# Performance work log

Measured on AMD Instinct MI355X. Metric: run time of the kernel, lower is better.

The kernel has to match this reference:

```python
import jax, jax.numpy as jnp
import numpy as np

NX, NY = 8, 1
IN_DELAY, FB_DELAY = 3, 3
MAX_DELAY = max(IN_DELAY, FB_DELAY)
HID = 64
NT, NG = 4096, 1024
IN_FEAT = (NX - NY) * (IN_DELAY + 1) + NY * (FB_DELAY + 1)  # 32


def setup_inputs() -> dict:
    key = jax.random.key(0)
    ks = jax.random.split(key, 10)
    s = lambda *sh: 0.05
    return {
        "x": jax.random.normal(ks[0], (NT, NG, NX), jnp.float32),
        "W_in": jax.random.normal(ks[1], (HID, IN_FEAT), jnp.float32) * 0.1,
        "b_in": jax.random.normal(ks[2], (HID,), jnp.float32) * 0.1,
        "W_ih": jax.random.normal(ks[3], (HID, HID), jnp.float32) * 0.1,
        "b_ih": jax.random.normal(ks[4], (HID,), jnp.float32) * 0.1,
        "W_hh": jax.random.normal(ks[5], (HID, HID), jnp.float32) * 0.1,
        "b_hh": jax.random.normal(ks[6], (HID,), jnp.float32) * 0.1,
        "W_out": jax.random.normal(ks[7], (NY, HID), jnp.float32) * 0.1,
        "b_out": jax.random.normal(ks[8], (NY,), jnp.float32) * 0.1,
    }


def _narx_forward(x, W_in, b_in, W_ih, b_ih, b_hh, W_out, b_out):
    nt = x.shape[0]
    # Source concat order: x0_t = x0[-1] then all x0[i], i=0..delay-1 (last slice duplicated).
    # x0 spans times [t-delay, t-1], so offsets relative to t are:
    off_x = jnp.array([-1] + list(range(-IN_DELAY, 0)))   # [4]
    off_y = jnp.array([-1] + list(range(-FB_DELAY, 0)))   # [4]
    ts = jnp.arange(MAX_DELAY, nt)                          # [T']
    # Gather delay windows: [T', n_off, ngrid, feat] -> [T', ngrid, n_off*feat]
    xw = x[ts[:, None] + off_x[None, :], :, :NX - NY]
    xw = jnp.transpose(xw, (0, 2, 1, 3)).reshape(xw.shape[0], xw.shape[2], -1)
    yw = x[ts[:, None] + off_y[None, :], :, NX - NY:]
    yw = jnp.transpose(yw, (0, 2, 1, 3)).reshape(yw.shape[0], yw.shape[2], -1)
    xt = jnp.concatenate([xw, yw], axis=-1)                 # [T', ngrid, IN_FEAT]
    h = jax.nn.relu(jnp.einsum('tgi,hi->tgh', xt, W_in) + b_in)
    # RNNCell called with hx=None each step in the source -> hidden is zeros every
    # call (W_hh contributes nothing); out = tanh(W_ih h + b_ih + b_hh).
    a = jnp.tanh(jnp.einsum('tgh,oh->tgo', h, W_ih) + b_ih + b_hh)
    y = jnp.einsum('tgh,oh->tgo', a, W_out) + b_out         # [T', ngrid, NY]
    # out[:max_delay] = x[:max_delay, :, -ny:]
    return jnp.concatenate([x[:MAX_DELAY, :, NX - NY:], y], axis=0)


def reference(x, W_in, b_in, W_ih, b_ih, W_hh, b_hh, W_out, b_out):
    # NestedNarx applies the shared Narx dl_model to every basin's series; with
    # the batched Narx this is exactly one call over all basins.
    return _narx_forward(x, W_in, b_in, W_ih, b_ih, b_hh, W_out, b_out)
```

## Files before the change

### kernel.cpp

```cpp
#include <hip/hip_runtime.h>
#include <hip/hip_bf16.h>


typedef __attribute__((ext_vector_type(8))) short bf16x8;
typedef __attribute__((ext_vector_type(4))) float f32x4;

__device__ __forceinline__ unsigned pk2(float lo, float hi) {
    __hip_bfloat162 h = __float22bfloat162_rn(float2{lo, hi});
    unsigned u; __builtin_memcpy(&u, &h, 4);
    return u;
}

union BF8 { bf16x8 v; unsigned u[4]; uint4 q; };


__global__ __launch_bounds__(64) void narx_prep(
    const float* __restrict__ W_in, const float* __restrict__ b_in,
    const float* __restrict__ W_ih, const float* __restrict__ b_ih,
    const float* __restrict__ b_hh, const float* __restrict__ W_out,
    uint4* __restrict__ ws)
{
    const int lane = threadIdx.x;
    const int c = lane >> 4, pl = lane & 15;

    #pragma unroll
    for (int T = 0; T < 4; ++T) {
        const int r = ((pl >> 2) * 8) + (pl & 3) + (T & 1) * 4 + (T >> 1) * 32;
        const float* W = W_in + r * 32;
        float wr[8];
        if (c == 0) {
            #pragma unroll
            for (int j = 0; j < 7; ++j) wr[j] = W[j] + W[21 + j];
            wr[7] = W[28] + W[31];
        } else if (c == 1) {
            #pragma unroll
            for (int j = 0; j < 7; ++j) wr[j] = W[14 + j];
            wr[7] = W[30];
        } else if (c == 2) {
            #pragma unroll
            for (int j = 0; j < 7; ++j) wr[j] = W[7 + j];
            wr[7] = W[29];
        } else {
            wr[0] = b_in[r];
            #pragma unroll
            for (int j = 1; j < 8; ++j) wr[j] = 0.0f;
        }
        BF8 t;
        t.u[0] = pk2(wr[0], wr[1]); t.u[1] = pk2(wr[2], wr[3]);
        t.u[2] = pk2(wr[4], wr[5]); t.u[3] = pk2(wr[6], wr[7]);
        ws[lane*4 + T] = t.q;
    }

    #pragma unroll
    for (int k0 = 0; k0 < 2; ++k0)
    #pragma unroll
    for (int U = 0; U < 4; ++U) {
        const int r = ((pl >> 2) * 8) + (pl & 3) + (U & 1) * 4 + (U >> 1) * 32;
        const float* p = W_ih + r * 64 + 32*k0 + 8*c;
        float4 u0 = *(const float4*)p, u1 = *(const float4*)(p + 4);
        BF8 t;
        t.u[0] = pk2(u0.x, u0.y); t.u[1] = pk2(u0.z, u0.w);
        t.u[2] = pk2(u1.x, u1.y); t.u[3] = pk2(u1.z, u1.w);
        ws[256 + lane*8 + k0*4 + U] = t.q;
    }

    float* bsum = (float*)&ws[1536];
    if (lane < 64) {  }
    float4* wsf = (float4*)ws;
    #pragma unroll
    for (int U = 0; U < 4; ++U) {
        const int o = 8*c + 4*(U & 1) + 32*(U >> 1);
        wsf[768 + lane*4 + U] = make_float4(b_ih[o+0]+b_hh[o+0], b_ih[o+1]+b_hh[o+1],
                                            b_ih[o+2]+b_hh[o+2], b_ih[o+3]+b_hh[o+3]);
    }
    (void)bsum;

    #pragma unroll
    for (int k0 = 0; k0 < 2; ++k0) {
        BF8 t;
        if (pl == 0) {
            const float* p = W_out + 32*k0 + 8*c;
            t.u[0] = pk2(p[0], p[1]); t.u[1] = pk2(p[2], p[3]);
            t.u[2] = pk2(p[4], p[5]); t.u[3] = pk2(p[6], p[7]);
        } else {
            t.u[0] = t.u[1] = t.u[2] = t.u[3] = 0u;
        }
        ws[1280 + lane*2 + k0] = t.q;
    }
}

__global__ __launch_bounds__(256, 2) void narx_main(
    const float* __restrict__ x, const uint4* __restrict__ ws,
    const float* __restrict__ b_out, float* __restrict__ out)
{
    __shared__ unsigned short F[4][128][32];

    const int nwg  = gridDim.x;
    const int orig = blockIdx.x;
    const int q8 = nwg >> 3, r8 = nwg & 7;
    const int xcd = orig & 7, inner = orig >> 3;
    const int b = (xcd < r8 ? xcd * (q8 + 1) : r8 * (q8 + 1) + (xcd - r8) * q8) + inner;

    const int lane = threadIdx.x & 63;
    const int w    = threadIdx.x >> 6;
    const int c    = lane >> 4;
    const int pl   = lane & 15;
    const int pt0  = 3072 + b * 512 + w * 128;

    bf16x8 wa[4];
    #pragma unroll
    for (int T = 0; T < 4; ++T) { BF8 t; t.q = ws[lane*4 + T]; wa[T] = t.v; }
    bf16x8 wi[2][4];
    #pragma unroll
    for (int k0 = 0; k0 < 2; ++k0)
    #pragma unroll
    for (int U = 0; U < 4; ++U) { BF8 t; t.q = ws[256 + lane*8 + k0*4 + U]; wi[k0][U] = t.v; }
    bf16x8 woa[2];
    #pragma unroll
    for (int k0 = 0; k0 < 2; ++k0) { BF8 t; t.q = ws[1280 + lane*2 + k0]; woa[k0] = t.v; }
    const float4* wsf = (const float4*)ws;
    f32x4 bias2[4];
    #pragma unroll
    for (int U = 0; U < 4; ++U) {
        float4 v = wsf[768 + lane*4 + U];
        bias2[U] = f32x4{v.x, v.y, v.z, v.w};
    }
    const float bout = b_out[0];
    const f32x4 cy = {c == 0 ? bout : 0.f, 0.f, 0.f, 0.f};
    const f32x4 zero = {0.f, 0.f, 0.f, 0.f};

    const float4* xr = (const float4*)x;
    {
        const int p0 = pt0 + lane, p1 = pt0 + 64 + lane;
        const int t0 = p0 >> 10, g0v = p0 & 1023;
        const int t1 = p1 >> 10, g1v = p1 & 1023;
        const size_t a1 = ((size_t)(t0-1)*1024 + g0v)*2, a2 = ((size_t)(t0-2)*1024 + g0v)*2,
                     a3 = ((size_t)(t0-3)*1024 + g0v)*2;
        const size_t d1a = ((size_t)(t1-1)*1024 + g1v)*2, d2a = ((size_t)(t1-2)*1024 + g1v)*2,
                     d3a = ((size_t)(t1-3)*1024 + g1v)*2;
        float4 A0 = xr[a1],  A1 = xr[a1+1],  B0 = xr[a2],  B1 = xr[a2+1],
               C0 = xr[a3],  C1 = xr[a3+1];
        float4 D0 = xr[d1a], D1 = xr[d1a+1], E0 = xr[d2a], E1 = xr[d2a+1],
               G0 = xr[d3a], G1 = xr[d3a+1];
        const int s = (lane >> 1) & 3;
        uint4* Fr0 = (uint4*)&F[w][lane][0];
        Fr0[0 ^ s] = make_uint4(pk2(A0.x,A0.y), pk2(A0.z,A0.w), pk2(A1.x,A1.y), pk2(A1.z,A1.w));
        Fr0[1 ^ s] = make_uint4(pk2(B0.x,B0.y), pk2(B0.z,B0.w), pk2(B1.x,B1.y), pk2(B1.z,B1.w));
        Fr0[2 ^ s] = make_uint4(pk2(C0.x,C0.y), pk2(C0.z,C0.w), pk2(C1.x,C1.y), pk2(C1.z,C1.w));
        Fr0[3 ^ s] = make_uint4(0x00003f80u, 0u, 0u, 0u);
        uint4* Fr1 = (uint4*)&F[w][64 + lane][0];
        Fr1[0 ^ s] = make_uint4(pk2(D0.x,D0.y), pk2(D0.z,D0.w), pk2(D1.x,D1.y), pk2(D1.z,D1.w));
        Fr1[1 ^ s] = make_uint4(pk2(E0.x,E0.y), pk2(E0.z,E0.w), pk2(E1.x,E1.y), pk2(E1.z,E1.w));
        Fr1[2 ^ s] = make_uint4(pk2(G0.x,G0.y), pk2(G0.z,G0.w), pk2(G1.x,G1.y), pk2(G1.z,G1.w));
        Fr1[3 ^ s] = make_uint4(0x00003f80u, 0u, 0u, 0u);
    }
    asm volatile("s_waitcnt lgkmcnt(0)" ::: "memory");
    __builtin_amdgcn_sched_barrier(0);

    asm volatile("" : "+v"(wa[0]), "+v"(wa[1]), "+v"(wa[2]), "+v"(wa[3]),
                      "+v"(wi[0][0]), "+v"(wi[0][1]), "+v"(wi[0][2]), "+v"(wi[0][3]),
                      "+v"(wi[1][0]), "+v"(wi[1][1]), "+v"(wi[1][2]), "+v"(wi[1][3]),
                      "+v"(bias2[0]), "+v"(bias2[1]), "+v"(bias2[2]), "+v"(bias2[3]),
                      "+v"(woa[0]), "+v"(woa[1]));

    const int s_rd = (pl >> 1) & 3;
    bf16x8 bf1 = *(bf16x8*)&F[w][pl][(c ^ s_rd) * 8];

    #pragma unroll 2
    for (int rb = 0; rb < 8; ++rb) {
        const int m0 = pt0 + rb * 16;

        f32x4 d1[4];
        #pragma unroll
        for (int T = 0; T < 4; ++T)
            d1[T] = __builtin_amdgcn_mfma_f32_16x16x32_bf16(wa[T], bf1, zero, 0, 0, 0);

        {
            const int rn = (rb < 7) ? rb + 1 : 7;
            bf1 = *(bf16x8*)&F[w][rn*16 + pl][(c ^ s_rd) * 8];
        }

        BF8 bh0, bh1;
        bh0.u[0] = pk2(fmaxf(d1[0][0],0.f), fmaxf(d1[0][1],0.f));
        bh0.u[1] = pk2(fmaxf(d1[0][2],0.f), fmaxf(d1[0][3],0.f));
        bh0.u[2] = pk2(fmaxf(d1[1][0],0.f), fmaxf(d1[1][1],0.f));
        bh0.u[3] = pk2(fmaxf(d1[1][2],0.f), fmaxf(d1[1][3],0.f));
        bh1.u[0] = pk2(fmaxf(d1[2][0],0.f), fmaxf(d1[2][1],0.f));
        bh1.u[1] = pk2(fmaxf(d1[2][2],0.f), fmaxf(d1[2][3],0.f));
        bh1.u[2] = pk2(fmaxf(d1[3][0],0.f), fmaxf(d1[3][1],0.f));
        bh1.u[3] = pk2(fmaxf(d1[3][2],0.f), fmaxf(d1[3][3],0.f));

        f32x4 d2[4];
        #pragma unroll
        for (int U = 0; U < 4; ++U) {
            d2[U] = __builtin_amdgcn_mfma_f32_16x16x32_bf16(wi[0][U], bh0.v, bias2[U], 0, 0, 0);
            d2[U] = __builtin_amdgcn_mfma_f32_16x16x32_bf16(wi[1][U], bh1.v, d2[U],   0, 0, 0);
        }

        f32x4 av[4];
        #pragma unroll
        for (int U = 0; U < 4; ++U) {
            f32x4 z;
            z[0] = __builtin_amdgcn_fmed3f(d2[U][0], -4.f, 4.f);
            z[1] = __builtin_amdgcn_fmed3f(d2[U][1], -4.f, 4.f);
            z[2] = __builtin_amdgcn_fmed3f(d2[U][2], -4.f, 4.f);
            z[3] = __builtin_amdgcn_fmed3f(d2[U][3], -4.f, 4.f);
            f32x4 p2  = z * z;
            f32x4 num = z * (p2 * (p2 + 105.f) + 945.f);
            f32x4 den = p2 * (p2 * 15.f + 420.f) + 945.f;
            f32x4 r;
            r[0] = __builtin_amdgcn_rcpf(den[0]);
            r[1] = __builtin_amdgcn_rcpf(den[1]);
            r[2] = __builtin_amdgcn_rcpf(den[2]);
            r[3] = __builtin_amdgcn_rcpf(den[3]);
            av[U] = num * r;
        }
        BF8 pb0, pb1;
        pb0.u[0] = pk2(av[0][0], av[0][1]); pb0.u[1] = pk2(av[0][2], av[0][3]);
        pb0.u[2] = pk2(av[1][0], av[1][1]); pb0.u[3] = pk2(av[1][2], av[1][3]);
        pb1.u[0] = pk2(av[2][0], av[2][1]); pb1.u[1] = pk2(av[2][2], av[2][3]);
        pb1.u[2] = pk2(av[3][0], av[3][1]); pb1.u[3] = pk2(av[3][2], av[3][3]);

        f32x4 dy;
        dy = __builtin_amdgcn_mfma_f32_16x16x32_bf16(woa[0], pb0.v, cy, 0, 0, 0);
        dy = __builtin_amdgcn_mfma_f32_16x16x32_bf16(woa[1], pb1.v, dy, 0, 0, 0);

        if (lane < 16)
            out[m0 + lane] = dy[0];
    }
}

__global__ __launch_bounds__(256) void narx_pass(const float* __restrict__ x, float* __restrict__ out) {
    const int i = blockIdx.x * 256 + threadIdx.x;
    out[i] = x[i * 8 + 7];
}

extern "C" void kernel_launch(void* const* d_in, const int* in_sizes, int n_in,
                              void* d_out, int out_size, void* d_ws, size_t ws_size,
                              hipStream_t stream) {
    const float* x     = (const float*)d_in[0];
    const float* W_in  = (const float*)d_in[1];
    const float* b_in  = (const float*)d_in[2];
    const float* W_ih  = (const float*)d_in[3];
    const float* b_ih  = (const float*)d_in[4];
    const float* b_hh  = (const float*)d_in[6];
    const float* W_out = (const float*)d_in[7];
    const float* b_out = (const float*)d_in[8];
    float* out = (float*)d_out;
    uint4* ws = (uint4*)d_ws;

    narx_prep<<<1, 64, 0, stream>>>(W_in, b_in, W_ih, b_ih, b_hh, W_out, ws);
    narx_main<<<8186, 256, 0, stream>>>(x, ws, b_out, out);
    narx_pass<<<12, 256, 0, stream>>>(x, out);
}
```

Baseline: 128.8 us.

## Load MFMA B-operands directly from global into registers, drop LDS staging; relu via abs trick

Removes the shared-memory staging buffer: each lane now loads its delayed-input slices straight from global memory into registers, software-prefetched four row-blocks ahead, and packs them into the bf16 B operand inline. ReLU is rewritten as 0.5*(h+|h|): W_ih is prescaled by 0.5 and the second layer runs twice as many MFMAs, once on h and once on |h|, replacing the max operations. Dropping LDS and raising the occupancy hint to 3 waves aims to hide latency better, at the cost of doubled second-layer matrix work and less coalesced, partly redundant global loads.

```diff
diff --git a/kernel.cpp b/kernel.cpp
--- a/kernel.cpp
+++ b/kernel.cpp
@@ -59,13 +59,11 @@
         const float* p = W_ih + r * 64 + 32*k0 + 8*c;
         float4 u0 = *(const float4*)p, u1 = *(const float4*)(p + 4);
         BF8 t;
-        t.u[0] = pk2(u0.x, u0.y); t.u[1] = pk2(u0.z, u0.w);
-        t.u[2] = pk2(u1.x, u1.y); t.u[3] = pk2(u1.z, u1.w);
+        t.u[0] = pk2(0.5f*u0.x, 0.5f*u0.y); t.u[1] = pk2(0.5f*u0.z, 0.5f*u0.w);
+        t.u[2] = pk2(0.5f*u1.x, 0.5f*u1.y); t.u[3] = pk2(0.5f*u1.z, 0.5f*u1.w);
         ws[256 + lane*8 + k0*4 + U] = t.q;
     }
 
-    float* bsum = (float*)&ws[1536];
-    if (lane < 64) {  }
     float4* wsf = (float4*)ws;
     #pragma unroll
     for (int U = 0; U < 4; ++U) {
@@ -73,7 +71,6 @@
         wsf[768 + lane*4 + U] = make_float4(b_ih[o+0]+b_hh[o+0], b_ih[o+1]+b_hh[o+1],
                                             b_ih[o+2]+b_hh[o+2], b_ih[o+3]+b_hh[o+3]);
     }
-    (void)bsum;
 
     #pragma unroll
     for (int k0 = 0; k0 < 2; ++k0) {
@@ -89,12 +86,10 @@
     }
 }
 
-__global__ __launch_bounds__(256, 2) void narx_main(
+__global__ __launch_bounds__(256, 3) void narx_main(
     const float* __restrict__ x, const uint4* __restrict__ ws,
     const float* __restrict__ b_out, float* __restrict__ out)
 {
-    __shared__ unsigned short F[4][128][32];
-
     const int nwg  = gridDim.x;
     const int orig = blockIdx.x;
     const int q8 = nwg >> 3, r8 = nwg & 7;
@@ -129,72 +124,68 @@
     const f32x4 cy = {c == 0 ? bout : 0.f, 0.f, 0.f, 0.f};
     const f32x4 zero = {0.f, 0.f, 0.f, 0.f};
 
-    const float4* xr = (const float4*)x;
-    {
-        const int p0 = pt0 + lane, p1 = pt0 + 64 + lane;
-        const int t0 = p0 >> 10, g0v = p0 & 1023;
-        const int t1 = p1 >> 10, g1v = p1 & 1023;
-        const size_t a1 = ((size_t)(t0-1)*1024 + g0v)*2, a2 = ((size_t)(t0-2)*1024 + g0v)*2,
-                     a3 = ((size_t)(t0-3)*1024 + g0v)*2;
-        const size_t d1a = ((size_t)(t1-1)*1024 + g1v)*2, d2a = ((size_t)(t1-2)*1024 + g1v)*2,
-                     d3a = ((size_t)(t1-3)*1024 + g1v)*2;
-        float4 A0 = xr[a1],  A1 = xr[a1+1],  B0 = xr[a2],  B1 = xr[a2+1],
-               C0 = xr[a3],  C1 = xr[a3+1];
-        float4 D0 = xr[d1a], D1 = xr[d1a+1], E0 = xr[d2a], E1 = xr[d2a+1],
-               G0 = xr[d3a], G1 = xr[d3a+1];
-        const int s = (lane >> 1) & 3;
-        uint4* Fr0 = (uint4*)&F[w][lane][0];
-        Fr0[0 ^ s] = make_uint4(pk2(A0.x,A0.y), pk2(A0.z,A0.w), pk2(A1.x,A1.y), pk2(A1.z,A1.w));
-        Fr0[1 ^ s] = make_uint4(pk2(B0.x,B0.y), pk2(B0.z,B0.w), pk2(B1.x,B1.y), pk2(B1.z,B1.w));
-        Fr0[2 ^ s] = make_uint4(pk2(C0.x,C0.y), pk2(C0.z,C0.w), pk2(C1.x,C1.y), pk2(C1.z,C1.w));
-        Fr0[3 ^ s] = make_uint4(0x00003f80u, 0u, 0u, 0u);
-        uint4* Fr1 = (uint4*)&F[w][64 + lane][0];
-        Fr1[0 ^ s] = make_uint4(pk2(D0.x,D0.y), pk2(D0.z,D0.w), pk2(D1.x,D1.y), pk2(D1.z,D1.w));
-        Fr1[1 ^ s] = make_uint4(pk2(E0.x,E0.y), pk2(E0.z,E0.w), pk2(E1.x,E1.y), pk2(E1.z,E1.w));
-        Fr1[2 ^ s] = make_uint4(pk2(G0.x,G0.y), pk2(G0.z,G0.w), pk2(G1.x,G1.y), pk2(G1.z,G1.w));
-        Fr1[3 ^ s] = make_uint4(0x00003f80u, 0u, 0u, 0u);
-    }
-    asm volatile("s_waitcnt lgkmcnt(0)" ::: "memory");
-    __builtin_amdgcn_sched_barrier(0);
-
     asm volatile("" : "+v"(wa[0]), "+v"(wa[1]), "+v"(wa[2]), "+v"(wa[3]),
                       "+v"(wi[0][0]), "+v"(wi[0][1]), "+v"(wi[0][2]), "+v"(wi[0][3]),
                       "+v"(wi[1][0]), "+v"(wi[1][1]), "+v"(wi[1][2]), "+v"(wi[1][3]),
                       "+v"(bias2[0]), "+v"(bias2[1]), "+v"(bias2[2]), "+v"(bias2[3]),
                       "+v"(woa[0]), "+v"(woa[1]));
 
-    const int s_rd = (pl >> 1) & 3;
-    bf16x8 bf1 = *(bf16x8*)&F[w][pl][(c ^ s_rd) * 8];
-
-    #pragma unroll 2
+    const int t  = pt0 >> 10, g0 = pt0 & 1023;
+    const int dly = (c < 3) ? c : 0;
+    const float* xb = x + ((size_t)(t - 1 - dly) * 1024 + g0 + pl) * 8;
+    float4 L0[4], L1[4];
+    if (c < 3) {
+        #pragma unroll
+        for (int i = 0; i < 4; ++i) {
+            const float4* p = (const float4*)(xb + i * 128);
+            L0[i] = p[0]; L1[i] = p[1];
+        }
+    }
+
+    #pragma unroll
     for (int rb = 0; rb < 8; ++rb) {
         const int m0 = pt0 + rb * 16;
 
+        bf16x8 bf1;
+        {
+            BF8 tv;
+            if (c < 3) {
+                float4 a = L0[rb & 3], bq = L1[rb & 3];
+                tv.u[0] = pk2(a.x, a.y);  tv.u[1] = pk2(a.z, a.w);
+                tv.u[2] = pk2(bq.x, bq.y); tv.u[3] = pk2(bq.z, bq.w);
+            } else {
+                tv.u[0] = 0x00003f80u; tv.u[1] = 0u; tv.u[2] = 0u; tv.u[3] = 0u;
+            }
+            bf1 = tv.v;
+        }
+
         f32x4 d1[4];
         #pragma unroll
         for (int T = 0; T < 4; ++T)
             d1[T] = __builtin_amdgcn_mfma_f32_16x16x32_bf16(wa[T], bf1, zero, 0, 0, 0);
 
-        {
-            const int rn = (rb < 7) ? rb + 1 : 7;
-            bf1 = *(bf16x8*)&F[w][rn*16 + pl][(c ^ s_rd) * 8];
-        }
-
-        BF8 bh0, bh1;
-        bh0.u[0] = pk2(fmaxf(d1[0][0],0.f), fmaxf(d1[0][1],0.f));
-        bh0.u[1] = pk2(fmaxf(d1[0][2],0.f), fmaxf(d1[0][3],0.f));
-        bh0.u[2] = pk2(fmaxf(d1[1][0],0.f), fmaxf(d1[1][1],0.f));
-        bh0.u[3] = pk2(fmaxf(d1[1][2],0.f), fmaxf(d1[1][3],0.f));
-        bh1.u[0] = pk2(fmaxf(d1[2][0],0.f), fmaxf(d1[2][1],0.f));
-        bh1.u[1] = pk2(fmaxf(d1[2][2],0.f), fmaxf(d1[2][3],0.f));
-        bh1.u[2] = pk2(fmaxf(d1[3][0],0.f), fmaxf(d1[3][1],0.f));
-        bh1.u[3] = pk2(fmaxf(d1[3][2],0.f), fmaxf(d1[3][3],0.f));
+        if (rb < 4 && c < 3) {
+            const float4* p = (const float4*)(xb + (rb + 4) * 128);
+            L0[rb & 3] = p[0]; L1[rb & 3] = p[1];
+        }
+
+        BF8 bh0, bh1, ba0, ba1;
+        bh0.u[0] = pk2(d1[0][0], d1[0][1]); bh0.u[1] = pk2(d1[0][2], d1[0][3]);
+        bh0.u[2] = pk2(d1[1][0], d1[1][1]); bh0.u[3] = pk2(d1[1][2], d1[1][3]);
+        bh1.u[0] = pk2(d1[2][0], d1[2][1]); bh1.u[1] = pk2(d1[2][2], d1[2][3]);
+        bh1.u[2] = pk2(d1[3][0], d1[3][1]); bh1.u[3] = pk2(d1[3][2], d1[3][3]);
+        ba0.u[0] = pk2(fabsf(d1[0][0]), fabsf(d1[0][1])); ba0.u[1] = pk2(fabsf(d1[0][2]), fabsf(d1[0][3]));
+        ba0.u[2] = pk2(fabsf(d1[1][0]), fabsf(d1[1][1])); ba0.u[3] = pk2(fabsf(d1[1][2]), fabsf(d1[1][3]));
+        ba1.u[0] = pk2(fabsf(d1[2][0]), fabsf(d1[2][1])); ba1.u[1] = pk2(fabsf(d1[2][2]), fabsf(d1[2][3]));
+        ba1.u[2] = pk2(fabsf(d1[3][0]), fabsf(d1[3][1])); ba1.u[3] = pk2(fabsf(d1[3][2]), fabsf(d1[3][3]));
 
         f32x4 d2[4];
         #pragma unroll
         for (int U = 0; U < 4; ++U) {
             d2[U] = __builtin_amdgcn_mfma_f32_16x16x32_bf16(wi[0][U], bh0.v, bias2[U], 0, 0, 0);
+            d2[U] = __builtin_amdgcn_mfma_f32_16x16x32_bf16(wi[0][U], ba0.v, d2[U],   0, 0, 0);
             d2[U] = __builtin_amdgcn_mfma_f32_16x16x32_bf16(wi[1][U], bh1.v, d2[U],   0, 0, 0);
+            d2[U] = __builtin_amdgcn_mfma_f32_16x16x32_bf16(wi[1][U], ba1.v, d2[U],   0, 0, 0);
         }
 
         f32x4 av[4];
```

Result: slower. 178.6 us (+38.6%).
